# Kernel tuning notes

Hardware: AMD Instinct MI355X
Metric: run time of the kernel (lower is better)

The kernel has to match this reference:

```python
import jax, jax.numpy as jnp
import numpy as np

H = 1024      # hidden_size
NH = 8        # num_attention_heads
HD = H // NH  # head dim = 128
FF = 3072     # DebertaConfig default intermediate_size
MAXPOS = 512  # max_position_embeddings
EPS = 1e-7    # DeBERTa layer_norm_eps


def layer_norm(x, g, b):
    m = jnp.mean(x, axis=-1, keepdims=True)
    v = jnp.mean((x - m) ** 2, axis=-1, keepdims=True)
    return (x - m) * jax.lax.rsqrt(v + EPS) * g + b


def setup_inputs() -> dict:
    key = jax.random.key(0)
    ks = jax.random.split(key, 12)
    s = 0.02  # init std
    B, S = 16, 512
    return {
        "x": jax.random.normal(ks[0], (B, S, H), jnp.float32),
        "pos_emb": jax.random.normal(ks[1], (MAXPOS, H), jnp.float32) * s,
        "emb_ln_g": jnp.ones((H,), jnp.float32),
        "emb_ln_b": jnp.zeros((H,), jnp.float32),
        "Wq": jax.random.normal(ks[2], (H, H), jnp.float32) * s,
        "Wk": jax.random.normal(ks[3], (H, H), jnp.float32) * s,
        "Wv": jax.random.normal(ks[4], (H, H), jnp.float32) * s,
        "q_bias": jax.random.normal(ks[5], (H,), jnp.float32) * s,
        "v_bias": jax.random.normal(ks[6], (H,), jnp.float32) * s,
        "Wo": jax.random.normal(ks[7], (H, H), jnp.float32) * s,
        "bo": jnp.zeros((H,), jnp.float32),
        "ln1_g": jnp.ones((H,), jnp.float32),
        "ln1_b": jnp.zeros((H,), jnp.float32),
        "Wi": jax.random.normal(ks[8], (H, FF), jnp.float32) * s,
        "bi": jnp.zeros((FF,), jnp.float32),
        "Wf": jax.random.normal(ks[9], (FF, H), jnp.float32) * s,
        "bf": jnp.zeros((H,), jnp.float32),
        "ln2_g": jnp.ones((H,), jnp.float32),
        "ln2_b": jnp.zeros((H,), jnp.float32),
    }


def reference(x, pos_emb, emb_ln_g, emb_ln_b, Wq, Wk, Wv, q_bias, v_bias,
              Wo, bo, ln1_g, ln1_b, Wi, bi, Wf, bf, ln2_g, ln2_b):
    B, S, _ = x.shape
    # DebertaEmbeddings: inputs_embeds + absolute position embeddings, LayerNorm (eval: no dropout)
    h = layer_norm(x + pos_emb[:S], emb_ln_g, emb_ln_b)
    # DisentangledSelfAttention with pos_att_type=[] -> standard attention, scale_factor=1;
    # in_proj has no bias, but q and v get learned bias vectors.
    q = (h @ Wq + q_bias).reshape(B, S, NH, HD).transpose(0, 2, 1, 3)  # [B,NH,S,HD]
    k = (h @ Wk).reshape(B, S, NH, HD).transpose(0, 2, 1, 3)
    v = (h @ Wv + v_bias).reshape(B, S, NH, HD).transpose(0, 2, 1, 3)
    scale = jnp.sqrt(jnp.asarray(HD, x.dtype))
    scores = jnp.einsum('bhqd,bhkd->bhqk', q / scale, k)  # [B,NH,S,S]
    probs = jax.nn.softmax(scores, axis=-1)  # attention_mask all ones -> plain softmax
    ctx = jnp.einsum('bhqk,bhkd->bhqd', probs, v)
    ctx = ctx.transpose(0, 2, 1, 3).reshape(B, S, H)
    # SelfOutput: dense + residual + LayerNorm
    attn_out = layer_norm(ctx @ Wo + bo + h, ln1_g, ln1_b)
    # Intermediate (exact gelu) + Output: dense + residual + LayerNorm
    ff = jax.nn.gelu(attn_out @ Wi + bi, approximate=False)
    out = layer_norm(ff @ Wf + bf + attn_out, ln2_g, ln2_b)
    return out
```

## Files before the change

### kernel.cpp

```cpp
#include <hip/hip_runtime.h>
#include <hip/hip_bf16.h>

#define BB  16
#define SS  512
#define HH  1024
#define NHH 8
#define HDD 128
#define FFF 3072
#define TT  (BB * SS)

typedef __hip_bfloat16 bf16;
typedef short s8v __attribute__((ext_vector_type(8)));
typedef float f4v __attribute__((ext_vector_type(4)));

__device__ __forceinline__ float bf2f(bf16 v) { return __bfloat162float(v); }
__device__ __forceinline__ bf16 f2bf(float f) { return __float2bfloat16(f); }
__device__ __forceinline__ float us2f(unsigned short u) {
  union { unsigned int i; float f; } c; c.i = (unsigned int)u << 16; return c.f;
}

__global__ void embed_ln_kernel(const float* __restrict__ x, const float* __restrict__ pos,
                                const float* __restrict__ g, const float* __restrict__ bta,
                                bf16* __restrict__ h) {
  int t = blockIdx.x;
  int s = t & (SS - 1);
  int tid = threadIdx.x;
  const float* xr = x + (size_t)t * HH;
  const float* pr = pos + (size_t)s * HH;
  float vals[4];
  float sum = 0.f;
#pragma unroll
  for (int i = 0; i < 4; i++) {
    int c = tid + i * 256;
    vals[i] = xr[c] + pr[c];
    sum += vals[i];
  }
  __shared__ float red[4];
#pragma unroll
  for (int off = 32; off > 0; off >>= 1) sum += __shfl_down(sum, off, 64);
  if ((tid & 63) == 0) red[tid >> 6] = sum;
  __syncthreads();
  float mean = (red[0] + red[1] + red[2] + red[3]) * (1.f / HH);
  float vsum = 0.f;
#pragma unroll
  for (int i = 0; i < 4; i++) { float d = vals[i] - mean; vsum += d * d; }
  __syncthreads();
#pragma unroll
  for (int off = 32; off > 0; off >>= 1) vsum += __shfl_down(vsum, off, 64);
  if ((tid & 63) == 0) red[tid >> 6] = vsum;
  __syncthreads();
  float rstd = rsqrtf((red[0] + red[1] + red[2] + red[3]) * (1.f / HH) + 1e-7f);
  bf16* hr = h + (size_t)t * HH;
#pragma unroll
  for (int i = 0; i < 4; i++) {
    int c = tid + i * 256;
    hr[c] = f2bf((vals[i] - mean) * rstd * g[c] + bta[c]);
  }
}

template <int OUT_F32>
__global__ void add_ln_kernel(const bf16* __restrict__ a, const bf16* __restrict__ res,
                              const float* __restrict__ g, const float* __restrict__ bta,
                              void* __restrict__ outv) {
  int t = blockIdx.x;
  int tid = threadIdx.x;
  const bf16* ar = a + (size_t)t * HH;
  const bf16* rr = res + (size_t)t * HH;
  float vals[4];
  float sum = 0.f;
#pragma unroll
  for (int i = 0; i < 4; i++) {
    int c = tid + i * 256;
    vals[i] = bf2f(ar[c]) + bf2f(rr[c]);
    sum += vals[i];
  }
  __shared__ float red[4];
#pragma unroll
  for (int off = 32; off > 0; off >>= 1) sum += __shfl_down(sum, off, 64);
  if ((tid & 63) == 0) red[tid >> 6] = sum;
  __syncthreads();
  float mean = (red[0] + red[1] + red[2] + red[3]) * (1.f / HH);
  float vsum = 0.f;
#pragma unroll
  for (int i = 0; i < 4; i++) { float d = vals[i] - mean; vsum += d * d; }
  __syncthreads();
#pragma unroll
  for (int off = 32; off > 0; off >>= 1) vsum += __shfl_down(vsum, off, 64);
  if ((tid & 63) == 0) red[tid >> 6] = vsum;
  __syncthreads();
  float rstd = rsqrtf((red[0] + red[1] + red[2] + red[3]) * (1.f / HH) + 1e-7f);
#pragma unroll
  for (int i = 0; i < 4; i++) {
    int c = tid + i * 256;
    float o = (vals[i] - mean) * rstd * g[c] + bta[c];
    if (OUT_F32)
      ((float*)outv)[(size_t)t * HH + c] = o;
    else
      ((bf16*)outv)[(size_t)t * HH + c] = f2bf(o);
  }
}

__global__ void convert_w_kernel(const float* __restrict__ W, bf16* __restrict__ Wt,
                                 int K, int N) {
  __shared__ float tile[32][33];
  int n0 = blockIdx.x * 32, k0 = blockIdx.y * 32;
#pragma unroll
  for (int it = 0; it < 4; it++) {
    int idx = threadIdx.x + it * 256;
    int ty = idx >> 5, tx = idx & 31;
    tile[ty][tx] = W[(size_t)(k0 + ty) * N + n0 + tx];
  }
  __syncthreads();
#pragma unroll
  for (int it = 0; it < 4; it++) {
    int idx = threadIdx.x + it * 256;
    int ty = idx >> 5, tx = idx & 31;
    Wt[(size_t)(n0 + ty) * K + k0 + tx] = f2bf(tile[tx][ty]);
  }
}

__global__ void build_qkv_bias_kernel(const float* __restrict__ qb,
                                      const float* __restrict__ vb,
                                      float* __restrict__ o) {
  int i = blockIdx.x * 256 + threadIdx.x;
  float v = 0.f;
  if (i < HH) v = qb[i];
  else if (i >= 2 * HH) v = vb[i - 2 * HH];
  o[i] = v;
}

__global__ void transpose_v_kernel(const bf16* __restrict__ v, bf16* __restrict__ vt) {
  __shared__ unsigned short tile[32][33];
  int bh = blockIdx.z;
  int s0 = blockIdx.x * 32, d0 = blockIdx.y * 32;
  int b = bh >> 3, hd = bh & 7;
  const unsigned short* vp = (const unsigned short*)v + ((size_t)b * SS) * (3 * HH) + hd * HDD;
  unsigned short* vtp = (unsigned short*)vt + (size_t)bh * HDD * SS;
#pragma unroll
  for (int it = 0; it < 4; it++) {
    int idx = threadIdx.x + it * 256;
    int ty = idx >> 5, tx = idx & 31;
    tile[ty][tx] = vp[(size_t)(s0 + ty) * (3 * HH) + d0 + tx];
  }
  __syncthreads();
#pragma unroll
  for (int it = 0; it < 4; it++) {
    int idx = threadIdx.x + it * 256;
    int ty = idx >> 5, tx = idx & 31;
    vtp[(size_t)(d0 + ty) * SS + s0 + tx] = tile[tx][ty];
  }
}

template <int GELU>
__global__ __launch_bounds__(256)
void mfma_gemm_kernel(const bf16* __restrict__ A, int lda, long long sAb, long long sAh,
                      const bf16* __restrict__ Bt, int ldb, long long sBb, long long sBh,
                      const float* __restrict__ bias,
                      bf16* __restrict__ C, int ldc, long long sCb, long long sCh,
                      int M, int N, int K, float scale) {
  __shared__ unsigned short Als[128 * 40];
  __shared__ unsigned short Bls[128 * 40];
  int tid = threadIdx.x;
  int lane = tid & 63, wave = tid >> 6;
  int l15 = lane & 15, quad = lane >> 4;
  int wm = wave & 1, wn = wave >> 1;
  int m0 = blockIdx.y * 128, n0 = blockIdx.x * 128;
  int zb = blockIdx.z >> 3, zh = blockIdx.z & 7;
  const bf16* Ab = A + zb * sAb + zh * sAh;
  const bf16* Bb = Bt + zb * sBb + zh * sBh;
  bf16* Cb = C + zb * sCb + zh * sCh;
  f4v acc[4][4];
#pragma unroll
  for (int i = 0; i < 4; i++)
#pragma unroll
    for (int j = 0; j < 4; j++) acc[i][j] = (f4v){0.f, 0.f, 0.f, 0.f};
  int r0 = tid >> 2;
  int q8 = (tid & 3) * 8;
  const bf16* Ap0 = Ab + (size_t)(m0 + r0) * lda + q8;
  const bf16* Ap1 = Ab + (size_t)(m0 + r0 + 64) * lda + q8;
  const bf16* Bp0 = Bb + (size_t)(n0 + r0) * ldb + q8;
  const bf16* Bp1 = Bb + (size_t)(n0 + r0 + 64) * ldb + q8;
  uint4 a0 = *(const uint4*)(Ap0);
  uint4 a1 = *(const uint4*)(Ap1);
  uint4 b0 = *(const uint4*)(Bp0);
  uint4 b1 = *(const uint4*)(Bp1);
  for (int k0 = 0; k0 < K; k0 += 32) {
    *(uint4*)&Als[r0 * 40 + q8] = a0;
    *(uint4*)&Als[(r0 + 64) * 40 + q8] = a1;
    *(uint4*)&Bls[r0 * 40 + q8] = b0;
    *(uint4*)&Bls[(r0 + 64) * 40 + q8] = b1;
    __syncthreads();
    int kn = k0 + 32;
    if (kn < K) {
      a0 = *(const uint4*)(Ap0 + kn);
      a1 = *(const uint4*)(Ap1 + kn);
      b0 = *(const uint4*)(Bp0 + kn);
      b1 = *(const uint4*)(Bp1 + kn);
    }
    s8v af[4], bfr[4];
#pragma unroll
    for (int i = 0; i < 4; i++)
      af[i] = *(const s8v*)&Als[(wm * 64 + i * 16 + l15) * 40 + quad * 8];
#pragma unroll
    for (int j = 0; j < 4; j++)
      bfr[j] = *(const s8v*)&Bls[(wn * 64 + j * 16 + l15) * 40 + quad * 8];
#pragma unroll
    for (int i = 0; i < 4; i++)
#pragma unroll
      for (int j = 0; j < 4; j++)
        acc[i][j] = __builtin_amdgcn_mfma_f32_16x16x32_bf16(af[i], bfr[j], acc[i][j], 0, 0, 0);
    __syncthreads();
  }
#pragma unroll
  for (int i = 0; i < 4; i++) {
#pragma unroll
    for (int j = 0; j < 4; j++) {
      int n = n0 + wn * 64 + j * 16 + l15;
      float bval = bias ? bias[n] : 0.f;
#pragma unroll
      for (int r = 0; r < 4; r++) {
        int m = m0 + wm * 64 + i * 16 + quad * 4 + r;
        float v = (acc[i][j][r] + bval) * scale;
        if (GELU) v = 0.5f * v * (1.f + erff(v * 0.70710678118654752f));
        Cb[(size_t)m * ldc + n] = f2bf(v);
      }
    }
  }
}

__global__ void softmax_kernel(bf16* __restrict__ sc) {
  int wave = threadIdx.x >> 6, lane = threadIdx.x & 63;
  size_t row = (size_t)blockIdx.x * 4 + wave;
  unsigned short* p = (unsigned short*)sc + row * SS + lane * 8;
  union { uint4 u4; unsigned short u[8]; } buf;
  buf.u4 = *(const uint4*)p;
  float v[8];
  float mx = -1e30f;
#pragma unroll
  for (int j = 0; j < 8; j++) { v[j] = us2f(buf.u[j]); mx = fmaxf(mx, v[j]); }
#pragma unroll
  for (int off = 32; off > 0; off >>= 1) mx = fmaxf(mx, __shfl_xor(mx, off));
  float sum = 0.f;
#pragma unroll
  for (int j = 0; j < 8; j++) { v[j] = __expf(v[j] - mx); sum += v[j]; }
#pragma unroll
  for (int off = 32; off > 0; off >>= 1) sum += __shfl_xor(sum, off);
  float inv = 1.f / sum;
  union { uint4 u4; unsigned short u[8]; } obuf;
#pragma unroll
  for (int j = 0; j < 8; j++) {
    bf16 b = f2bf(v[j] * inv);
    obuf.u[j] = *(unsigned short*)&b;
  }
  *(uint4*)p = obuf.u4;
}

extern "C" void kernel_launch(void* const* d_in, const int* in_sizes, int n_in,
                              void* d_out, int out_size, void* d_ws, size_t ws_size,
                              hipStream_t stream) {
  const float* x     = (const float*)d_in[0];
  const float* pos   = (const float*)d_in[1];
  const float* eg    = (const float*)d_in[2];
  const float* ebeta = (const float*)d_in[3];
  const float* Wq    = (const float*)d_in[4];
  const float* Wk    = (const float*)d_in[5];
  const float* Wv    = (const float*)d_in[6];
  const float* qbias = (const float*)d_in[7];
  const float* vbias = (const float*)d_in[8];
  const float* Wo    = (const float*)d_in[9];
  const float* bo    = (const float*)d_in[10];
  const float* l1g   = (const float*)d_in[11];
  const float* l1b   = (const float*)d_in[12];
  const float* Wi    = (const float*)d_in[13];
  const float* bi    = (const float*)d_in[14];
  const float* Wf    = (const float*)d_in[15];
  const float* bfb   = (const float*)d_in[16];
  const float* l2g   = (const float*)d_in[17];
  const float* l2b   = (const float*)d_in[18];

  char* w = (char*)d_ws;
  const size_t MB = (size_t)1 << 20;
  bf16* h      = (bf16*)(w + 0 * MB);
  bf16* qkv    = (bf16*)(w + 16 * MB);
  bf16* ctx    = (bf16*)(w + 64 * MB);
  bf16* tmp1   = (bf16*)(w + 80 * MB);
  bf16* attn   = (bf16*)(w + 96 * MB);
  bf16* scores = (bf16*)(w + 112 * MB);
  bf16* ff     = (bf16*)(w + 112 * MB);
  bf16* tmp2   = (bf16*)(w + 176 * MB);
  bf16* vt     = (bf16*)(w + 192 * MB);
  bf16* Wqkvt  = (bf16*)(w + 208 * MB);
  bf16* Wot    = (bf16*)(w + 214 * MB);
  bf16* Wit    = (bf16*)(w + 216 * MB);
  bf16* Wft    = (bf16*)(w + 222 * MB);
  float* qkvb  = (float*)(w + 228 * MB);
  float* out   = (float*)d_out;

  const float QSCALE = 0.08838834764831845f;

  embed_ln_kernel<<<TT, 256, 0, stream>>>(x, pos, eg, ebeta, h);

  convert_w_kernel<<<dim3(HH / 32, HH / 32), 256, 0, stream>>>(Wq, Wqkvt, HH, HH);
  convert_w_kernel<<<dim3(HH / 32, HH / 32), 256, 0, stream>>>(Wk, Wqkvt + (size_t)HH * HH, HH, HH);
  convert_w_kernel<<<dim3(HH / 32, HH / 32), 256, 0, stream>>>(Wv, Wqkvt + (size_t)2 * HH * HH, HH, HH);
  convert_w_kernel<<<dim3(HH / 32, HH / 32), 256, 0, stream>>>(Wo, Wot, HH, HH);
  convert_w_kernel<<<dim3(FFF / 32, HH / 32), 256, 0, stream>>>(Wi, Wit, HH, FFF);
  convert_w_kernel<<<dim3(HH / 32, FFF / 32), 256, 0, stream>>>(Wf, Wft, FFF, HH);
  build_qkv_bias_kernel<<<12, 256, 0, stream>>>(qbias, vbias, qkvb);

  mfma_gemm_kernel<0><<<dim3(24, 64, 1), 256, 0, stream>>>(
      h, HH, 0, 0, Wqkvt, HH, 0, 0, qkvb, qkv, 3 * HH, 0, 0, TT, 3 * HH, HH, 1.f);

  mfma_gemm_kernel<0><<<dim3(4, 4, BB * NHH), 256, 0, stream>>>(
      qkv, 3 * HH, (long long)SS * 3 * HH, HDD,
      qkv + HH, 3 * HH, (long long)SS * 3 * HH, HDD,
      nullptr,
      scores, SS, (long long)NHH * SS * SS, (long long)SS * SS,
      SS, SS, HDD, QSCALE);

  softmax_kernel<<<BB * NHH * SS / 4, 256, 0, stream>>>(scores);

  transpose_v_kernel<<<dim3(SS / 32, HDD / 32, BB * NHH), 256, 0, stream>>>(qkv + 2 * HH, vt);

  mfma_gemm_kernel<0><<<dim3(1, 4, BB * NHH), 256, 0, stream>>>(
      scores, SS, (long long)NHH * SS * SS, (long long)SS * SS,
      vt, SS, (long long)NHH * HDD * SS, (long long)HDD * SS,
      nullptr,
      ctx, HH, (long long)SS * HH, HDD,
      SS, HDD, SS, 1.f);

  mfma_gemm_kernel<0><<<dim3(8, 64, 1), 256, 0, stream>>>(
      ctx, HH, 0, 0, Wot, HH, 0, 0, bo, tmp1, HH, 0, 0, TT, HH, HH, 1.f);
  add_ln_kernel<0><<<TT, 256, 0, stream>>>(tmp1, h, l1g, l1b, attn);

  mfma_gemm_kernel<1><<<dim3(24, 64, 1), 256, 0, stream>>>(
      attn, HH, 0, 0, Wit, HH, 0, 0, bi, ff, FFF, 0, 0, TT, FFF, HH, 1.f);
  mfma_gemm_kernel<0><<<dim3(8, 64, 1), 256, 0, stream>>>(
      ff, FFF, 0, 0, Wft, FFF, 0, 0, bfb, tmp2, HH, 0, 0, TT, HH, FFF, 1.f);
  add_ln_kernel<1><<<TT, 256, 0, stream>>>(tmp2, attn, l2g, l2b, out);
}
```

Measured before the change: 531.8 us.

## Fuse QK^T, softmax and PV into one attention kernel; swizzle GEMM LDS

Replaces the separate scores GEMM, softmax kernel and PV GEMM with one fused attention kernel per (32-query tile, batch-head). That kernel keeps the full 32x512 score row block in LDS, so the bf16 score matrix never goes to HBM. Normalization is deferred to the output using per-row inverse sums. Separately, the generic GEMM's LDS layout drops its padding for an XOR swizzle, meant to avoid bank conflicts while using less LDS. The fused kernel uses about 45KB of LDS and a small 32-row M tile, which may limit occupancy and MFMA efficiency.

```diff
diff --git a/kernel.cpp b/kernel.cpp
--- a/kernel.cpp
+++ b/kernel.cpp
@@ -158,8 +158,8 @@
                       const float* __restrict__ bias,
                       bf16* __restrict__ C, int ldc, long long sCb, long long sCh,
                       int M, int N, int K, float scale) {
-  __shared__ unsigned short Als[128 * 40];
-  __shared__ unsigned short Bls[128 * 40];
+  __shared__ __align__(16) unsigned short Als[128 * 32];
+  __shared__ __align__(16) unsigned short Bls[128 * 32];
   int tid = threadIdx.x;
   int lane = tid & 63, wave = tid >> 6;
   int l15 = lane & 15, quad = lane >> 4;
@@ -176,6 +176,10 @@
     for (int j = 0; j < 4; j++) acc[i][j] = (f4v){0.f, 0.f, 0.f, 0.f};
   int r0 = tid >> 2;
   int q8 = (tid & 3) * 8;
+  int fw = (r0 >> 1) & 3;
+  int wlo = r0 * 32 + (((tid & 3) ^ fw) * 8);
+  int whi = (r0 + 64) * 32 + (((tid & 3) ^ fw) * 8);
+  int qx = (quad ^ ((l15 >> 1) & 3)) * 8;
   const bf16* Ap0 = Ab + (size_t)(m0 + r0) * lda + q8;
   const bf16* Ap1 = Ab + (size_t)(m0 + r0 + 64) * lda + q8;
   const bf16* Bp0 = Bb + (size_t)(n0 + r0) * ldb + q8;
@@ -185,10 +189,10 @@
   uint4 b0 = *(const uint4*)(Bp0);
   uint4 b1 = *(const uint4*)(Bp1);
   for (int k0 = 0; k0 < K; k0 += 32) {
-    *(uint4*)&Als[r0 * 40 + q8] = a0;
-    *(uint4*)&Als[(r0 + 64) * 40 + q8] = a1;
-    *(uint4*)&Bls[r0 * 40 + q8] = b0;
-    *(uint4*)&Bls[(r0 + 64) * 40 + q8] = b1;
+    *(uint4*)&Als[wlo] = a0;
+    *(uint4*)&Als[whi] = a1;
+    *(uint4*)&Bls[wlo] = b0;
+    *(uint4*)&Bls[whi] = b1;
     __syncthreads();
     int kn = k0 + 32;
     if (kn < K) {
@@ -200,10 +204,10 @@
     s8v af[4], bfr[4];
 #pragma unroll
     for (int i = 0; i < 4; i++)
-      af[i] = *(const s8v*)&Als[(wm * 64 + i * 16 + l15) * 40 + quad * 8];
+      af[i] = *(const s8v*)&Als[(wm * 64 + i * 16 + l15) * 32 + qx];
 #pragma unroll
     for (int j = 0; j < 4; j++)
-      bfr[j] = *(const s8v*)&Bls[(wn * 64 + j * 16 + l15) * 40 + quad * 8];
+      bfr[j] = *(const s8v*)&Bls[(wn * 64 + j * 16 + l15) * 32 + qx];
 #pragma unroll
     for (int i = 0; i < 4; i++)
 #pragma unroll
@@ -228,31 +232,136 @@
   }
 }
 
-__global__ void softmax_kernel(bf16* __restrict__ sc) {
-  int wave = threadIdx.x >> 6, lane = threadIdx.x & 63;
-  size_t row = (size_t)blockIdx.x * 4 + wave;
-  unsigned short* p = (unsigned short*)sc + row * SS + lane * 8;
-  union { uint4 u4; unsigned short u[8]; } buf;
-  buf.u4 = *(const uint4*)p;
-  float v[8];
-  float mx = -1e30f;
-#pragma unroll
-  for (int j = 0; j < 8; j++) { v[j] = us2f(buf.u[j]); mx = fmaxf(mx, v[j]); }
-#pragma unroll
-  for (int off = 32; off > 0; off >>= 1) mx = fmaxf(mx, __shfl_xor(mx, off));
-  float sum = 0.f;
-#pragma unroll
-  for (int j = 0; j < 8; j++) { v[j] = __expf(v[j] - mx); sum += v[j]; }
-#pragma unroll
-  for (int off = 32; off > 0; off >>= 1) sum += __shfl_xor(sum, off);
-  float inv = 1.f / sum;
-  union { uint4 u4; unsigned short u[8]; } obuf;
-#pragma unroll
-  for (int j = 0; j < 8; j++) {
-    bf16 b = f2bf(v[j] * inv);
-    obuf.u[j] = *(unsigned short*)&b;
-  }
-  *(uint4*)p = obuf.u4;
+__global__ __launch_bounds__(256)
+void fused_attn_kernel(const bf16* __restrict__ qkv, const bf16* __restrict__ vt,
+                       bf16* __restrict__ ctx) {
+  __shared__ __align__(16) unsigned short Qs[32 * 136];
+  __shared__ __align__(16) unsigned short St[128 * 40];
+  __shared__ __align__(16) unsigned short P[32 * 520];
+  __shared__ float invs[32];
+  const float QSCALE = 0.08838834764831845f;
+  int tid = threadIdx.x;
+  int lane = tid & 63, wave = tid >> 6;
+  int l15 = lane & 15, quad = lane >> 4;
+  int wm = wave & 1, wn = wave >> 1;
+  int qt = blockIdx.x;
+  int bh = blockIdx.y;
+  int b = bh >> 3, hd = bh & 7;
+  size_t rowQ = (size_t)b * SS + qt * 32;
+
+  {
+    int r = tid >> 4, ck = (tid & 15) * 8;
+    *(uint4*)&Qs[r * 136 + ck] =
+        *(const uint4*)(qkv + (rowQ + r) * (3 * HH) + hd * HDD + ck);
+    *(uint4*)&Qs[(r + 16) * 136 + ck] =
+        *(const uint4*)(qkv + (rowQ + r + 16) * (3 * HH) + hd * HDD + ck);
+  }
+
+  int r0 = tid >> 2;
+  int q8 = (tid & 3) * 8;
+  f4v acc[4];
+#pragma unroll
+  for (int j = 0; j < 4; j++) acc[j] = (f4v){0.f, 0.f, 0.f, 0.f};
+
+#define KSRC(tt, rr) (qkv + ((size_t)b * SS + ((tt) >> 2) * 128 + (rr)) * (3 * HH) \
+                          + HH + hd * HDD + ((tt) & 3) * 32 + q8)
+  uint4 ka = *(const uint4*)KSRC(0, r0);
+  uint4 kb = *(const uint4*)KSRC(0, r0 + 64);
+  for (int tt = 0; tt < 16; ++tt) {
+    *(uint4*)&St[r0 * 40 + q8] = ka;
+    *(uint4*)&St[(r0 + 64) * 40 + q8] = kb;
+    __syncthreads();
+    if (tt < 15) {
+      ka = *(const uint4*)KSRC(tt + 1, r0);
+      kb = *(const uint4*)KSRC(tt + 1, r0 + 64);
+    }
+    int kt = tt & 3;
+    s8v af = *(const s8v*)&Qs[(wm * 16 + l15) * 136 + kt * 32 + quad * 8];
+    s8v bfr[4];
+#pragma unroll
+    for (int j = 0; j < 4; j++)
+      bfr[j] = *(const s8v*)&St[(wn * 64 + j * 16 + l15) * 40 + quad * 8];
+#pragma unroll
+    for (int j = 0; j < 4; j++)
+      acc[j] = __builtin_amdgcn_mfma_f32_16x16x32_bf16(af, bfr[j], acc[j], 0, 0, 0);
+    __syncthreads();
+    if (kt == 3) {
+      int nt = tt >> 2;
+#pragma unroll
+      for (int j = 0; j < 4; j++)
+#pragma unroll
+        for (int r = 0; r < 4; r++)
+          P[(wm * 16 + quad * 4 + r) * 520 + nt * 128 + wn * 64 + j * 16 + l15] =
+              (unsigned short)__bfloat16_as_ushort(f2bf(acc[j][r] * QSCALE));
+#pragma unroll
+      for (int j = 0; j < 4; j++) acc[j] = (f4v){0.f, 0.f, 0.f, 0.f};
+    }
+  }
+#undef KSRC
+
+  __syncthreads();
+  {
+    int row = tid >> 3, sub = tid & 7;
+    uint4* pp = (uint4*)&P[row * 520 + sub * 64];
+    float mx = -1e30f;
+#pragma unroll
+    for (int c = 0; c < 8; c++) {
+      union { uint4 u4; unsigned short u[8]; } w; w.u4 = pp[c];
+#pragma unroll
+      for (int e = 0; e < 8; e++) mx = fmaxf(mx, us2f(w.u[e]));
+    }
+    mx = fmaxf(mx, __shfl_xor(mx, 1));
+    mx = fmaxf(mx, __shfl_xor(mx, 2));
+    mx = fmaxf(mx, __shfl_xor(mx, 4));
+    float sum = 0.f;
+#pragma unroll
+    for (int c = 0; c < 8; c++) {
+      union { uint4 u4; unsigned short u[8]; } w; w.u4 = pp[c];
+#pragma unroll
+      for (int e = 0; e < 8; e++) {
+        float f = __expf(us2f(w.u[e]) - mx);
+        sum += f;
+        bf16 bb = f2bf(f);
+        w.u[e] = *(unsigned short*)&bb;
+      }
+      pp[c] = w.u4;
+    }
+    sum += __shfl_xor(sum, 1);
+    sum += __shfl_xor(sum, 2);
+    sum += __shfl_xor(sum, 4);
+    if (sub == 0) invs[row] = 1.f / sum;
+  }
+
+  const bf16* vb = vt + (size_t)bh * HDD * SS;
+  uint4 va0 = *(const uint4*)(vb + (size_t)r0 * SS + q8);
+  uint4 va1 = *(const uint4*)(vb + (size_t)(r0 + 64) * SS + q8);
+  for (int kt = 0; kt < 16; ++kt) {
+    *(uint4*)&St[r0 * 40 + q8] = va0;
+    *(uint4*)&St[(r0 + 64) * 40 + q8] = va1;
+    __syncthreads();
+    if (kt < 15) {
+      va0 = *(const uint4*)(vb + (size_t)r0 * SS + (kt + 1) * 32 + q8);
+      va1 = *(const uint4*)(vb + (size_t)(r0 + 64) * SS + (kt + 1) * 32 + q8);
+    }
+    s8v af = *(const s8v*)&P[(wm * 16 + l15) * 520 + kt * 32 + quad * 8];
+    s8v bfr[4];
+#pragma unroll
+    for (int j = 0; j < 4; j++)
+      bfr[j] = *(const s8v*)&St[(wn * 64 + j * 16 + l15) * 40 + quad * 8];
+#pragma unroll
+    for (int j = 0; j < 4; j++)
+      acc[j] = __builtin_amdgcn_mfma_f32_16x16x32_bf16(af, bfr[j], acc[j], 0, 0, 0);
+    __syncthreads();
+  }
+#pragma unroll
+  for (int j = 0; j < 4; j++) {
+#pragma unroll
+    for (int r = 0; r < 4; r++) {
+      int rl = wm * 16 + quad * 4 + r;
+      int d = wn * 64 + j * 16 + l15;
+      ctx[(rowQ + rl) * HH + hd * HDD + d] = f2bf(acc[j][r] * invs[rl]);
+    }
+  }
 }
 
 extern "C" void kernel_launch(void* const* d_in, const int* in_sizes, int n_in,
@@ -285,7 +394,6 @@
   bf16* ctx    = (bf16*)(w + 64 * MB);
   bf16* tmp1   = (bf16*)(w + 80 * MB);
   bf16* attn   = (bf16*)(w + 96 * MB);
-  bf16* scores = (bf16*)(w + 112 * MB);
   bf16* ff     = (bf16*)(w + 112 * MB);
   bf16* tmp2   = (bf16*)(w + 176 * MB);
   bf16* vt     = (bf16*)(w + 192 * MB);
@@ -296,8 +404,6 @@
   float* qkvb  = (float*)(w + 228 * MB);
   float* out   = (float*)d_out;
 
-  const float QSCALE = 0.08838834764831845f;
-
   embed_ln_kernel<<<TT, 256, 0, stream>>>(x, pos, eg, ebeta, h);
 
   convert_w_kernel<<<dim3(HH / 32, HH / 32), 256, 0, stream>>>(Wq, Wqkvt, HH, HH);
@@ -311,23 +417,9 @@
   mfma_gemm_kernel<0><<<dim3(24, 64, 1), 256, 0, stream>>>(
       h, HH, 0, 0, Wqkvt, HH, 0, 0, qkvb, qkv, 3 * HH, 0, 0, TT, 3 * HH, HH, 1.f);
 
-  mfma_gemm_kernel<0><<<dim3(4, 4, BB * NHH), 256, 0, stream>>>(
-      qkv, 3 * HH, (long long)SS * 3 * HH, HDD,
-      qkv + HH, 3 * HH, (long long)SS * 3 * HH, HDD,
-      nullptr,
-      scores, SS, (long long)NHH * SS * SS, (long long)SS * SS,
-      SS, SS, HDD, QSCALE);
-
-  softmax_kernel<<<BB * NHH * SS / 4, 256, 0, stream>>>(scores);
-
   transpose_v_kernel<<<dim3(SS / 32, HDD / 32, BB * NHH), 256, 0, stream>>>(qkv + 2 * HH, vt);
 
-  mfma_gemm_kernel<0><<<dim3(1, 4, BB * NHH), 256, 0, stream>>>(
-      scores, SS, (long long)NHH * SS * SS, (long long)SS * SS,
-      vt, SS, (long long)NHH * HDD * SS, (long long)HDD * SS,
-      nullptr,
-      ctx, HH, (long long)SS * HH, HDD,
-      SS, HDD, SS, 1.f);
+  fused_attn_kernel<<<dim3(SS / 32, BB * NHH), 256, 0, stream>>>(qkv, vt, ctx);
 
   mfma_gemm_kernel<0><<<dim3(8, 64, 1), 256, 0, stream>>>(
       ctx, HH, 0, 0, Wot, HH, 0, 0, bo, tmp1, HH, 0, 0, TT, HH, HH, 1.f);
```

New measurement: 536.8 us. Within noise of the previous version (+0.9%).
